# Performance work log

Hardware: AMD Instinct MI355X
Metric: run time of the kernel (lower is better)

## Reference

```python
import jax, jax.numpy as jnp
import numpy as np

N, C_IN, T, V = 64, 64, 64, 25
C_OUT = 64
DK = DV = 16
NH = 8
DKH, DVH = DK // NH, DV // NH
KT = 9
EPS = 1e-5


def make_pe(channel, joint_num, time_len):
    # temporal positional encoding: position index = frame id, repeated per joint
    pos = np.repeat(np.arange(time_len), joint_num).astype(np.float32)[:, None]
    pe = np.zeros((time_len * joint_num, channel), np.float32)
    div = np.exp(np.arange(0, channel, 2).astype(np.float32) * -(np.log(10000.0) / channel))
    pe[:, 0::2] = np.sin(pos * div)
    pe[:, 1::2] = np.cos(pos * div)
    return jnp.asarray(pe.reshape(time_len, joint_num, channel).transpose(2, 0, 1)[None])  # (1,C,time,joint)


def setup_inputs():
    key = jax.random.key(0)
    ks = jax.random.split(key, 17)
    rn = lambda k, s, sc=0.05: jax.random.normal(k, s, jnp.float32) * sc
    return {
        'x': jax.random.normal(ks[0], (N, C_IN, T, V), jnp.float32),
        'pe': make_pe(C_IN, V, 64),
        'data_bn_g': 1.0 + rn(ks[1], (C_IN * V,)),
        'data_bn_b': rn(ks[2], (C_IN * V,)),
        'qkv_w': rn(ks[3], (3 * DK + DV, C_IN), 0.1),
        'qkv_b': rn(ks[4], (3 * DK + DV,)),
        'attn_w': rn(ks[5], (DV, DV), 0.1),
        'attn_b': rn(ks[6], (DV,)),
        'tcn_w': rn(ks[7], (C_OUT - DV, C_IN, KT, 1), 0.05),
        'tcn_b': rn(ks[8], (C_OUT - DV,)),
        'tcn_bn_g': 1.0 + rn(ks[9], (C_OUT - DV,)),
        'tcn_bn_b': rn(ks[10], (C_OUT - DV,)),
        'fc1_w': rn(ks[11], (C_OUT // 2, C_OUT), 0.1),
        'fc1_b': rn(ks[12], (C_OUT // 2,)),
        'fc2_w': rn(ks[13], (C_OUT, C_OUT // 2), 0.1),
        'fc2_b': rn(ks[14], (C_OUT,)),
        'bn_g': 1.0 + rn(ks[15], (C_OUT,)),
        'bn_b': rn(ks[16], (C_OUT,)),
    }


def _bn_eval(x, g, b, axis=1):
    # eval-mode BatchNorm with running_mean=0, running_var=1
    shape = [1] * x.ndim
    shape[axis] = -1
    scale = g / jnp.sqrt(1.0 + EPS)
    return x * scale.reshape(shape) + b.reshape(shape)


def _qkv_heads(x2d, qkv_w, qkv_b):
    # x2d: (B, C, T); 1x1 conv == channel matmul; split q/k/g/v, g is projected but unused
    qkv = jnp.einsum('oc,bct->bot', qkv_w, x2d) + qkv_b[None, :, None]
    q, k, _g, v = jnp.split(qkv, [DK, 2 * DK, 3 * DK], axis=1)
    B = x2d.shape[0]
    split = lambda z, ch: z.reshape(B, NH, ch // NH, -1)  # (B, Nh, chh, T)
    q = split(q, DK) * (DKH ** -0.5)
    return q, split(k, DK), split(v, DV)


def reference(x, pe, data_bn_g, data_bn_b, qkv_w, qkv_b, attn_w, attn_b,
              tcn_w, tcn_b, tcn_bn_g, tcn_bn_b, fc1_w, fc1_b, fc2_w, fc2_b, bn_g, bn_b):
    y = x + pe[:, :, :T]                                 # positional encoding (N,C,T,V)
    x_sum = x
    # data_bn over flattened (C*V) channels
    xb = x.transpose(0, 1, 3, 2).reshape(N, C_IN * V, T)
    xb = _bn_eval(xb, data_bn_g, data_bn_b)
    xn = xb.reshape(N, C_IN, V, T).transpose(0, 1, 3, 2)  # (N,C,T,V)
    # fold joints into batch: (N*V, C, T)
    xf = xn.transpose(0, 3, 1, 2).reshape(N * V, C_IN, T)
    yf = y.transpose(0, 3, 1, 2).reshape(N * V, C_IN, T)
    fq, fk, fv = _qkv_heads(xf, qkv_w, qkv_b)
    pq, pk, _ = _qkv_heads(yf, qkv_w, qkv_b)
    mu_q = fq.mean(-1, keepdims=True)                     # (B,H,dkh,1)
    fqc = fq - mu_q
    logits_pos = jnp.einsum('bhcs,bhct->bhst', pq, pk)    # (B,H,T,T)
    pairwise = jnp.einsum('bhcs,bhct->bhst', fqc, fk)     # (B,H,T,T)
    unary = jnp.einsum('bhcs,bhct->bhst', mu_q, fk)       # (B,H,1,T)
    weights = jnp.tanh(pairwise + logits_pos) + jnp.tanh(unary + logits_pos)
    ao = jnp.einsum('bhst,bhct->bhsc', weights, fv)       # (B,H,T,dvh)
    # (B,H,1,T,dvh) -> permute(0,1,4,2,3) -> combine heads -> (B, DV, T)
    ao = ao.transpose(0, 1, 3, 2).reshape(N * V, DV, T)
    ao = jnp.einsum('oc,bct->bot', attn_w, ao) + attn_b[None, :, None]
    ao = ao.reshape(N, V, DV, T).transpose(0, 2, 3, 1)    # (N, DV, T, V)
    # temporal conv branch (Unit2D: conv(k=9 temporal) + eval BN)
    tc = jax.lax.conv_general_dilated(x_sum, tcn_w, (1, 1), ((KT // 2, KT // 2), (0, 0)),
                                      dimension_numbers=('NCHW', 'OIHW', 'NCHW'))
    tc = tc + tcn_b[None, :, None, None]
    tc = _bn_eval(tc, tcn_bn_g, tcn_bn_b)
    result = jnp.concatenate([tc, ao], axis=1) + x_sum    # residual (down is None)
    # SE-style channel gating
    se = result.mean(axis=(2, 3))                         # (N, C_OUT)
    gate = jax.nn.sigmoid(jax.nn.relu(se @ fc1_w.T + fc1_b) @ fc2_w.T + fc2_b)
    result = result * gate[:, :, None, None] + result
    result = _bn_eval(result, bn_g, bn_b)
    return jax.nn.relu(result)
```

## Files before the change

kernel.cpp:

```cpp
#include <hip/hip_runtime.h>
#include <hip/hip_bf16.h>
#include <math.h>

#define TV_ 1600
#define SCALE_K 2.885390081777927f
#define RS2_ 0.70710678118654752f

typedef __attribute__((ext_vector_type(8))) short bf16x8;
typedef __attribute__((ext_vector_type(4))) float f32x4;
typedef __attribute__((ext_vector_type(2))) __fp16 h2f;

__device__ __forceinline__ float tanh_scaled(float y) {
    y = fminf(44.f, fmaxf(-44.f, y));
    float e = __builtin_amdgcn_exp2f(y);
    float r = __builtin_amdgcn_rcpf(e + 1.f);
    return __builtin_fmaf(e, r, -r);
}

__device__ __forceinline__ ushort f2bf(float f) {
    __hip_bfloat16 h = __float2bfloat16(f);
    return *(ushort*)&h;
}
__device__ __forceinline__ float bf2f(ushort u) {
    uint w = ((uint)u) << 16;
    return __uint_as_float(w);
}

__global__ __launch_bounds__(256) void t1_kernel(
    const float* __restrict__ x, const float* __restrict__ pe,
    const float* __restrict__ tcn_w, const float* __restrict__ tg,
    const float* __restrict__ qkv_w, const float* __restrict__ qkv_b,
    ushort* __restrict__ rt, float* __restrict__ Sbuf, float* __restrict__ Tt,
    ushort* __restrict__ wb, ushort* __restrict__ wq, float* __restrict__ qb,
    ushort* __restrict__ pet)
{
    const int tid = threadIdx.x;
    const int bx = blockIdx.x, by = blockIdx.y;

    if (bx == 25) {
        #pragma unroll 1
        for (int j = 0; j < 9; ++j) {
            int idx = by * 256 + tid + j * 16384;
            if (idx < 27648) {
                int oc = idx / 576, kk = idx - oc * 576;
                int kt = kk >> 6, ci = kk & 63;
                float a = tg[oc] * rsqrtf(1.f + 1e-5f);
                wb[idx] = f2bf(tcn_w[(oc * 64 + ci) * 9 + kt] * a);
            } else if (idx < 32768) {
                int i2 = idx - 27648;
                int r = i2 >> 6, c = i2 & 63;
                int src; float sc;
                if (r < 16)      { src = r;      sc = RS2_; }
                else if (r < 32) { src = r;      sc = SCALE_K; }
                else if (r < 48) { src = r + 16; sc = 1.f; }
                else if (r < 64) { src = r - 48; sc = RS2_; }
                else             { src = r - 48; sc = SCALE_K; }
                wq[i2] = f2bf(qkv_w[src * 64 + c] * sc);
            } else if (idx < 32848) {
                int r = idx - 32768;
                int src; float sc;
                if (r < 16)      { src = r;      sc = RS2_; }
                else if (r < 32) { src = r;      sc = SCALE_K; }
                else if (r < 48) { src = r + 16; sc = 1.f; }
                else if (r < 64) { src = r - 48; sc = RS2_; }
                else             { src = r - 48; sc = SCALE_K; }
                qb[r] = qkv_b[src] * sc;
            } else if (idx < 135248) {
                int i3 = idx - 32848;
                int ci = i3 / 1600, tv = i3 - ci * 1600;
                pet[tv * 64 + ci] = f2bf(pe[ci * 1600 + tv]);
            }
        }
        return;
    }
    if (bx == 26) {
        const int n = by;
        #pragma unroll
        for (int it = 0; it < 2; ++it) {
            int item = tid + it * 256;
            int ci = item >> 3, slot = item & 7;
            int t = (slot < 4) ? slot : (56 + slot);
            const float* xp = x + (n * 64 + ci) * TV_ + t * 25;
            float s = 0.f;
            #pragma unroll
            for (int v = 0; v < 25; ++v) s += xp[v];
            Tt[(n * 64 + ci) * 8 + slot] = s;
        }
        return;
    }

    __shared__ ushort smt[64 * 66];
    const int tv0 = bx * 64;
    const int n = by;
    const int tvl = tid & 63, cig = tid >> 6;
    const int tv = tv0 + tvl;

    float psum[16];
    #pragma unroll
    for (int k = 0; k < 16; ++k) psum[k] = 0.f;
    #pragma unroll
    for (int k = 0; k < 16; ++k) {
        int ci = k * 4 + cig;
        float xv = x[(n * 64 + ci) * TV_ + tv];
        smt[tvl * 66 + ci] = f2bf(xv);
        psum[k] += xv;
    }
    #pragma unroll
    for (int k = 0; k < 16; ++k) {
        float s = psum[k];
        #pragma unroll
        for (int off = 32; off >= 1; off >>= 1) s += __shfl_down(s, off, 64);
        if (tvl == 0) atomicAdd(&Sbuf[n * 64 + k * 4 + cig], s);
    }
    __syncthreads();

    #pragma unroll
    for (int j = 0; j < 8; ++j) {
        int chunk = tid + j * 256;
        int tvr = chunk >> 5, p = chunk & 31;
        uint val = *(const uint*)&smt[tvr * 66 + p * 2];
        *(uint*)&rt[(n * TV_ + tv0 + tvr) * 64 + p * 2] = val;
    }
}

__global__ __launch_bounds__(256, 5) void score_kernel(
    const ushort* __restrict__ rt, const ushort* __restrict__ pet,
    const float* __restrict__ dbg, const float* __restrict__ dbb,
    const ushort* __restrict__ wq, const float* __restrict__ qb,
    const float* __restrict__ attn_w, const float* __restrict__ attn_b,
    float* __restrict__ aoc, float* __restrict__ se)
{
    __shared__ float sm[5312];
    ushort* smu = (ushort*)sm;
    const int MU_ = 1056, AO = 1120;
    const int FKP = 2400, PKP = 2976, FVP = 3552, PQP = 4128, FQP = 4704;

    const int b = blockIdx.x;
    const int l = b >> 3;
    const int n = (b & 7) * 8 + l / 25;
    const int v = l % 25;
    const int tid = threadIdx.x;

    const int lane = tid & 63, wave = tid >> 6;
    const int m16 = lane & 15, q = lane >> 4;

    {
        const int part = tid & 7;
        const int ci0 = part * 8;
        const float rs = rsqrtf(1.f + 1e-5f);
        float sc8[8], sh8[8];
        #pragma unroll
        for (int i = 0; i < 8; ++i) {
            sc8[i] = dbg[(ci0 + i) * 25 + v] * rs;
            sh8[i] = dbb[(ci0 + i) * 25 + v];
        }
        #pragma unroll
        for (int j = 0; j < 2; ++j) {
            int t = (tid + j * 256) >> 3;
            uint4 xr = *(const uint4*)&rt[(n * TV_ + t * 25 + v) * 64 + ci0];
            uint4 pr = *(const uint4*)&pet[(t * 25 + v) * 64 + ci0];
            const ushort* xu = (const ushort*)&xr;
            const ushort* pu = (const ushort*)&pr;
            ushort xs[8], ys[8];
            #pragma unroll
            for (int i = 0; i < 8; ++i) {
                float xf = bf2f(xu[i]);
                xs[i] = f2bf(xf * sc8[i] + sh8[i]);
                ys[i] = f2bf(xf + bf2f(pu[i]));
            }
            *(uint4*)&smu[t * 72 + ci0] = *(uint4*)xs;
            *(uint4*)&smu[4608 + t * 72 + ci0] = *(uint4*)ys;
        }
    }
    __syncthreads();

    f32x4 acc[5];
    #pragma unroll
    for (int mt = 0; mt < 5; ++mt) acc[mt] = (f32x4){0.f, 0.f, 0.f, 0.f};
    #pragma unroll
    for (int kt = 0; kt < 2; ++kt) {
        const int koff = kt * 32 + q * 8;
        bf16x8 bx = *(const bf16x8*)&smu[(wave * 16 + m16) * 72 + koff];
        bf16x8 by = *(const bf16x8*)&smu[4608 + (wave * 16 + m16) * 72 + koff];
        #pragma unroll
        for (int mt = 0; mt < 5; ++mt) {
            bf16x8 a = *(const bf16x8*)&wq[(mt * 16 + m16) * 64 + koff];
            acc[mt] = __builtin_amdgcn_mfma_f32_16x16x32_bf16(a, (mt < 3) ? bx : by, acc[mt], 0, 0, 0);
        }
    }
    __syncthreads();

    {
        const int t = wave * 16 + m16;
        #pragma unroll
        for (int r = 0; r < 4; ++r)
            sm[(q * 4 + r) * 66 + t] = acc[0][r] + qb[q * 4 + r];
        *(h2f*)&sm[FKP + t * 9 + 2 * q] =
            __builtin_amdgcn_cvt_pkrtz(acc[1][0] + qb[16 + q * 4], acc[1][1] + qb[16 + q * 4 + 1]);
        *(h2f*)&sm[FKP + t * 9 + 2 * q + 1] =
            __builtin_amdgcn_cvt_pkrtz(acc[1][2] + qb[16 + q * 4 + 2], acc[1][3] + qb[16 + q * 4 + 3]);
        *(h2f*)&sm[FVP + t * 9 + 2 * q] =
            __builtin_amdgcn_cvt_pkrtz(acc[2][0] + qb[32 + q * 4], acc[2][1] + qb[32 + q * 4 + 1]);
        *(h2f*)&sm[FVP + t * 9 + 2 * q + 1] =
            __builtin_amdgcn_cvt_pkrtz(acc[2][2] + qb[32 + q * 4 + 2], acc[2][3] + qb[32 + q * 4 + 3]);
        *(h2f*)&sm[PQP + t * 9 + 2 * q] =
            __builtin_amdgcn_cvt_pkrtz(acc[3][0] + qb[48 + q * 4], acc[3][1] + qb[48 + q * 4 + 1]);
        *(h2f*)&sm[PQP + t * 9 + 2 * q + 1] =
            __builtin_amdgcn_cvt_pkrtz(acc[3][2] + qb[48 + q * 4 + 2], acc[3][3] + qb[48 + q * 4 + 3]);
        *(h2f*)&sm[PKP + t * 9 + 2 * q] =
            __builtin_amdgcn_cvt_pkrtz(acc[4][0] + qb[64 + q * 4], acc[4][1] + qb[64 + q * 4 + 1]);
        *(h2f*)&sm[PKP + t * 9 + 2 * q + 1] =
            __builtin_amdgcn_cvt_pkrtz(acc[4][2] + qb[64 + q * 4 + 2], acc[4][3] + qb[64 + q * 4 + 3]);
    }
    __syncthreads();

    if (tid < 64) {
        int ch = tid & 15, qq = tid >> 4;
        float s = 0.f;
        #pragma unroll
        for (int t = 0; t < 16; ++t) s += sm[ch * 66 + qq * 16 + t];
        sm[MU_ + qq * 16 + ch] = s;
    }
    __syncthreads();
    if (tid < 16) {
        float mval = (sm[MU_ + tid] + sm[MU_ + 16 + tid] + sm[MU_ + 32 + tid] + sm[MU_ + 48 + tid]) * (1.f / 64.f);
        sm[MU_ + tid] = mval;
    }
    __syncthreads();

    #pragma unroll
    for (int e = 0; e < 2; ++e) {
        int idx = tid * 2 + e;
        int s = idx >> 3, h = idx & 7;
        float a = sm[(2 * h) * 66 + s] - sm[MU_ + 2 * h];
        float c = sm[(2 * h + 1) * 66 + s] - sm[MU_ + 2 * h + 1];
        *(h2f*)&sm[FQP + s * 9 + h] = __builtin_amdgcn_cvt_pkrtz(a, c);
    }
    __syncthreads();

    const int g3 = tid & 7, m3 = tid >> 3;
    #pragma unroll 1
    for (int h = 0; h < 8; ++h) {
        const float mu0 = sm[MU_ + 2 * h], mu1 = sm[MU_ + 2 * h + 1];
        float fq0c[2], fq1c[2], pq0[2], pq1[2];
        #pragma unroll
        for (int js = 0; js < 2; ++js) {
            int s = 2 * m3 + js;
            h2f fq2 = *(const h2f*)&sm[FQP + s * 9 + h];
            h2f pq2 = *(const h2f*)&sm[PQP + s * 9 + h];
            fq0c[js] = (float)fq2.x; fq1c[js] = (float)fq2.y;
            pq0[js] = (float)pq2.x;  pq1[js] = (float)pq2.y;
        }
        float ao00 = 0.f, ao01 = 0.f, ao10 = 0.f, ao11 = 0.f;
        #pragma unroll
        for (int ch = 0; ch < 2; ++ch) {
            float fk0[4], fk1[4], pk0[4], pk1[4], fv0[4], fv1[4], un[4];
            #pragma unroll
            for (int j = 0; j < 4; ++j) {
                int t = 8 * g3 + ch * 4 + j;
                h2f fk2 = *(const h2f*)&sm[FKP + t * 9 + h];
                h2f pk2 = *(const h2f*)&sm[PKP + t * 9 + h];
                h2f fv2 = *(const h2f*)&sm[FVP + t * 9 + h];
                fk0[j] = (float)fk2.x; fk1[j] = (float)fk2.y;
                pk0[j] = (float)pk2.x; pk1[j] = (float)pk2.y;
                fv0[j] = (float)fv2.x; fv1[j] = (float)fv2.y;
                un[j] = mu0 * fk0[j] + mu1 * fk1[j];
            }
            #pragma unroll
            for (int js = 0; js < 2; ++js) {
                #pragma unroll
                for (int j = 0; j < 4; ++j) {
                    float lp = pq0[js] * pk0[j] + pq1[js] * pk1[j];
                    float a1 = fq0c[js] * fk0[j] + fq1c[js] * fk1[j] + lp;
                    float a2 = un[j] + lp;
                    float w = tanh_scaled(a1) + tanh_scaled(a2);
                    if (js == 0) { ao00 += w * fv0[j]; ao01 += w * fv1[j]; }
                    else         { ao10 += w * fv0[j]; ao11 += w * fv1[j]; }
                }
            }
        }
        #pragma unroll
        for (int off = 1; off <= 4; off <<= 1) {
            ao00 += __shfl_xor(ao00, off);
            ao01 += __shfl_xor(ao01, off);
            ao10 += __shfl_xor(ao10, off);
            ao11 += __shfl_xor(ao11, off);
        }
        if (g3 == 0) {
            sm[AO + (2 * m3) * 20 + 2 * h]         = ao00;
            sm[AO + (2 * m3) * 20 + 2 * h + 1]     = ao01;
            sm[AO + (2 * m3 + 1) * 20 + 2 * h]     = ao10;
            sm[AO + (2 * m3 + 1) * 20 + 2 * h + 1] = ao11;
        }
    }
    __syncthreads();

    const int t = tid & 63, oq = tid >> 6;
    float aorow[16];
    #pragma unroll
    for (int i = 0; i < 4; ++i)
        *(float4*)&aorow[i * 4] = *(const float4*)&sm[AO + t * 20 + i * 4];
    float* aop = aoc + (n * 25 + v) * 1024;
    #pragma unroll
    for (int j = 0; j < 4; ++j) {
        int o = oq * 4 + j;
        float acc4 = attn_b[o];
        #pragma unroll
        for (int c = 0; c < 16; ++c) acc4 += attn_w[o * 16 + c] * aorow[c];
        aop[o * 64 + t] = acc4;
        float ssum = acc4;
        #pragma unroll
        for (int off = 32; off >= 1; off >>= 1) ssum += __shfl_down(ssum, off, 64);
        if ((tid & 63) == 0) atomicAdd(&se[n * 64 + 48 + o], ssum);
    }
}

__global__ __launch_bounds__(64) void gate_kernel(
    const float* __restrict__ se, const float* __restrict__ Sbuf,
    const float* __restrict__ Tt, const ushort* __restrict__ wb,
    const float* __restrict__ tcn_b, const float* __restrict__ tg,
    const float* __restrict__ tb,
    const float* __restrict__ fc1w, const float* __restrict__ fc1b,
    const float* __restrict__ fc2w, const float* __restrict__ fc2b,
    float* __restrict__ gate)
{
    const int n = blockIdx.x;
    const int tid = threadIdx.x;
    __shared__ float U[64][9], seL[64], hid[32];
    const float rs = rsqrtf(1.f + 1e-5f);

    {
        int ci = tid;
        float S = Sbuf[n * 64 + ci];
        float T[8];
        #pragma unroll
        for (int j = 0; j < 8; ++j) T[j] = Tt[(n * 64 + ci) * 8 + j];
        U[ci][0] = S - (T[4] + T[5] + T[6] + T[7]);
        U[ci][1] = S - (T[5] + T[6] + T[7]);
        U[ci][2] = S - (T[6] + T[7]);
        U[ci][3] = S - T[7];
        U[ci][4] = S;
        U[ci][5] = S - T[0];
        U[ci][6] = S - (T[0] + T[1]);
        U[ci][7] = S - (T[0] + T[1] + T[2]);
        U[ci][8] = S - (T[0] + T[1] + T[2] + T[3]);
    }
    __syncthreads();

    if (tid < 48) {
        int oc = tid;
        float cs = 0.f;
        #pragma unroll 1
        for (int kt = 0; kt < 9; ++kt) {
            #pragma unroll
            for (int cb = 0; cb < 8; ++cb) {
                bf16x8 w8 = *(const bf16x8*)&wb[oc * 576 + kt * 64 + cb * 8];
                #pragma unroll
                for (int i = 0; i < 8; ++i)
                    cs += bf2f((ushort)w8[i]) * U[cb * 8 + i][kt];
            }
        }
        float a = tg[oc] * rs;
        float cb_ = tcn_b[oc] * a + tb[oc];
        seL[oc] = (a * cs + 1600.f * cb_ + Sbuf[n * 64 + oc]) * (1.f / 1600.f);
    } else {
        seL[tid] = (se[n * 64 + tid] + Sbuf[n * 64 + tid]) * (1.f / 1600.f);
    }
    __syncthreads();
    if (tid < 32) {
        float a = fc1b[tid];
        #pragma unroll
        for (int c = 0; c < 64; ++c) a += fc1w[tid * 64 + c] * seL[c];
        hid[tid] = fmaxf(a, 0.f);
    }
    __syncthreads();
    float g = fc2b[tid];
    #pragma unroll
    for (int j = 0; j < 32; ++j) g += fc2w[tid * 32 + j] * hid[j];
    gate[n * 64 + tid] = 1.f / (1.f + __expf(-g));
}

__global__ __launch_bounds__(512, 1) void tcn_mfma_kernel(
    const ushort* __restrict__ rt, const float* __restrict__ x,
    const ushort* __restrict__ wb,
    const float* __restrict__ tcn_b, const float* __restrict__ tg,
    const float* __restrict__ tb, const float* __restrict__ gate,
    const float* __restrict__ bng, const float* __restrict__ bnb,
    float* __restrict__ out)
{
    __shared__ ushort xsl[600 * 72];
    const int b = blockIdx.x;
    const int n = b >> 2, tile = b & 3;
    const int t0 = tile * 16;
    const int tid = threadIdx.x;

    const int tvbase = (t0 - 4) * 25;
    for (int idx = tid; idx < 4800; idx += 512) {
        int r = idx >> 3, part = idx & 7;
        int tv = tvbase + r;
        uint4 val = make_uint4(0u, 0u, 0u, 0u);
        if (tv >= 0 && tv < TV_) val = *(const uint4*)&rt[(n * TV_ + tv) * 64 + part * 8];
        *(uint4*)&xsl[r * 72 + part * 8] = val;
    }
    __syncthreads();

    const int lane = tid & 63, wave = tid >> 6;
    const int m16 = lane & 15, q = lane >> 4;
    const int nt0 = wave * 3;

    f32x4 acc[3][3];
    f32x4 acc24[3];
    #pragma unroll
    for (int i = 0; i < 3; ++i)
        #pragma unroll
        for (int mt = 0; mt < 3; ++mt)
            acc[i][mt] = (f32x4){0.f, 0.f, 0.f, 0.f};
    #pragma unroll
    for (int mt = 0; mt < 3; ++mt) acc24[mt] = (f32x4){0.f, 0.f, 0.f, 0.f};

    for (int ktile = 0; ktile < 18; ++ktile) {
        const int kt = ktile >> 1;
        const int cib = (ktile & 1) * 32 + q * 8;
        bf16x8 afr[3];
        #pragma unroll
        for (int mt = 0; mt < 3; ++mt)
            afr[mt] = *(const bf16x8*)&wb[(mt * 16 + m16) * 576 + ktile * 32 + q * 8];
        #pragma unroll
        for (int i = 0; i < 3; ++i) {
            int p = (nt0 + i) * 16 + m16;
            bf16x8 bfr = *(const bf16x8*)&xsl[(p + kt * 25) * 72 + cib];
            #pragma unroll
            for (int mt = 0; mt < 3; ++mt)
                acc[i][mt] = __builtin_amdgcn_mfma_f32_16x16x32_bf16(afr[mt], bfr, acc[i][mt], 0, 0, 0);
        }
        if (wave == 0) {
            int p = 24 * 16 + m16;
            bf16x8 bfr = *(const bf16x8*)&xsl[(p + kt * 25) * 72 + cib];
            #pragma unroll
            for (int mt = 0; mt < 3; ++mt)
                acc24[mt] = __builtin_amdgcn_mfma_f32_16x16x32_bf16(afr[mt], bfr, acc24[mt], 0, 0, 0);
        }
    }

    const float rsbn = rsqrtf(1.f + 1e-5f);
    float cb3[3][4], m3_[3][4], bb3[3][4];
    #pragma unroll
    for (int mt = 0; mt < 3; ++mt)
        #pragma unroll
        for (int r = 0; r < 4; ++r) {
            int oc = mt * 16 + q * 4 + r;
            float a = tg[oc] * rsbn;
            cb3[mt][r] = tcn_b[oc] * a + tb[oc];
            m3_[mt][r] = (1.f + gate[n * 64 + oc]) * (bng[oc] * rsbn);
            bb3[mt][r] = bnb[oc];
        }
    #pragma unroll
    for (int i = 0; i < 3; ++i) {
        int posg = tile * 400 + (nt0 + i) * 16 + m16;
        #pragma unroll
        for (int mt = 0; mt < 3; ++mt) {
            #pragma unroll
            for (int r = 0; r < 4; ++r) {
                int oc = mt * 16 + q * 4 + r;
                float val = acc[i][mt][r] + cb3[mt][r] + x[(n * 64 + oc) * TV_ + posg];
                out[(n * 64 + oc) * TV_ + posg] = fmaxf(val * m3_[mt][r] + bb3[mt][r], 0.f);
            }
        }
    }
    if (wave == 0) {
        int posg = tile * 400 + 24 * 16 + m16;
        #pragma unroll
        for (int mt = 0; mt < 3; ++mt) {
            #pragma unroll
            for (int r = 0; r < 4; ++r) {
                int oc = mt * 16 + q * 4 + r;
                float val = acc24[mt][r] + cb3[mt][r] + x[(n * 64 + oc) * TV_ + posg];
                out[(n * 64 + oc) * TV_ + posg] = fmaxf(val * m3_[mt][r] + bb3[mt][r], 0.f);
            }
        }
    }
}

__global__ __launch_bounds__(256) void final_kernel(
    float* __restrict__ out, const float* __restrict__ aoc,
    const float* __restrict__ x, const float* __restrict__ gate,
    const float* __restrict__ bng, const float* __restrict__ bnb)
{
    const float rs = rsqrtf(1.f + 1e-5f);
    int idx = blockIdx.x * 256 + threadIdx.x;
    int n = idx / 6400;
    int rem = idx - n * 6400;
    int o = rem / 400, r4 = rem - o * 400;

    float4 val;
    const float* ap = aoc + (n * 25) * 1024 + o * 64;
    #pragma unroll
    for (int e = 0; e < 4; ++e) {
        int pos = r4 * 4 + e;
        int t = pos / 25, v = pos - t * 25;
        ((float*)&val)[e] = ap[v * 1024 + t];
    }
    int g4 = (n * 64 + 48 + o) * 400 + r4;
    float4 xr = ((const float4*)x)[g4];
    float mm = (1.f + gate[n * 64 + 48 + o]) * (bng[48 + o] * rs);
    float bb = bnb[48 + o];
    val.x = fmaxf((val.x + xr.x) * mm + bb, 0.f);
    val.y = fmaxf((val.y + xr.y) * mm + bb, 0.f);
    val.z = fmaxf((val.z + xr.z) * mm + bb, 0.f);
    val.w = fmaxf((val.w + xr.w) * mm + bb, 0.f);
    ((float4*)out)[g4] = val;
}

extern "C" void kernel_launch(void* const* d_in, const int* in_sizes, int n_in,
                              void* d_out, int out_size, void* d_ws, size_t ws_size,
                              hipStream_t stream) {
    const float* x     = (const float*)d_in[0];
    const float* pe    = (const float*)d_in[1];
    const float* dbg   = (const float*)d_in[2];
    const float* dbb   = (const float*)d_in[3];
    const float* qkvw  = (const float*)d_in[4];
    const float* qkvb  = (const float*)d_in[5];
    const float* attnw = (const float*)d_in[6];
    const float* attnb = (const float*)d_in[7];
    const float* tcnw  = (const float*)d_in[8];
    const float* tcnb  = (const float*)d_in[9];
    const float* tcng  = (const float*)d_in[10];
    const float* tcnbb = (const float*)d_in[11];
    const float* fc1w  = (const float*)d_in[12];
    const float* fc1b  = (const float*)d_in[13];
    const float* fc2w  = (const float*)d_in[14];
    const float* fc2b  = (const float*)d_in[15];
    const float* bng   = (const float*)d_in[16];
    const float* bnb   = (const float*)d_in[17];

    float* out  = (float*)d_out;
    float* se   = (float*)d_ws;
    float* Sbuf = se + 4096;
    float* Tt   = Sbuf + 4096;
    float* gate = Tt + 32768;
    float* qb   = gate + 4096;
    float* aoc  = qb + 96;
    ushort* wb  = (ushort*)(aoc + 1638400);
    ushort* wq  = wb + 27648;
    ushort* pet = wq + 5120;
    ushort* rt  = pet + 102400;

    hipMemsetAsync(se, 0, (4096 + 4096) * sizeof(float), stream);
    t1_kernel<<<dim3(27, 64), dim3(256), 0, stream>>>(
        x, pe, tcnw, tcng, qkvw, qkvb, rt, Sbuf, Tt, wb, wq, qb, pet);
    score_kernel<<<dim3(1600), dim3(256), 0, stream>>>(rt, pet, dbg, dbb, wq, qb, attnw, attnb, aoc, se);
    gate_kernel<<<dim3(64), dim3(64), 0, stream>>>(
        se, Sbuf, Tt, wb, tcnb, tcng, tcnbb, fc1w, fc1b, fc2w, fc2b, gate);
    tcn_mfma_kernel<<<dim3(256), dim3(512), 0, stream>>>(
        rt, x, wb, tcnb, tcng, tcnbb, gate, bng, bnb, out);
    final_kernel<<<dim3(1600), dim3(256), 0, stream>>>(out, aoc, x, gate, bng, bnb);
}
```

Measured before the change: 226.0 us.

## Fuse SE gate computation into TCN kernel and stage attention output through LDS

Removes the separate gate_kernel launch by computing the SE gate redundantly inside each tcn_mfma block, splitting the 48x9 weight dot products across 432 threads, with tile 0 writing the gate out for the final kernel. The final kernel now handles one (n, channel) pair per block and first loads the aoc rows coalesced into shared memory before transposing, replacing strided global gathers. The score kernel's occupancy hint is raised from 5 to 6. This trades one launch and uncoalesced reads for four-fold redundant gate work per sample and extra LDS use in the TCN kernel.

```diff
diff --git a/kernel.cpp b/kernel.cpp
--- a/kernel.cpp
+++ b/kernel.cpp
@@ -123,7 +123,7 @@
     }
 }
 
-__global__ __launch_bounds__(256, 5) void score_kernel(
+__global__ __launch_bounds__(256, 6) void score_kernel(
     const ushort* __restrict__ rt, const ushort* __restrict__ pet,
     const float* __restrict__ dbg, const float* __restrict__ dbb,
     const ushort* __restrict__ wq, const float* __restrict__ qb,
@@ -315,84 +315,28 @@
     }
 }
 
-__global__ __launch_bounds__(64) void gate_kernel(
-    const float* __restrict__ se, const float* __restrict__ Sbuf,
-    const float* __restrict__ Tt, const ushort* __restrict__ wb,
-    const float* __restrict__ tcn_b, const float* __restrict__ tg,
-    const float* __restrict__ tb,
-    const float* __restrict__ fc1w, const float* __restrict__ fc1b,
-    const float* __restrict__ fc2w, const float* __restrict__ fc2b,
-    float* __restrict__ gate)
-{
-    const int n = blockIdx.x;
-    const int tid = threadIdx.x;
-    __shared__ float U[64][9], seL[64], hid[32];
-    const float rs = rsqrtf(1.f + 1e-5f);
-
-    {
-        int ci = tid;
-        float S = Sbuf[n * 64 + ci];
-        float T[8];
-        #pragma unroll
-        for (int j = 0; j < 8; ++j) T[j] = Tt[(n * 64 + ci) * 8 + j];
-        U[ci][0] = S - (T[4] + T[5] + T[6] + T[7]);
-        U[ci][1] = S - (T[5] + T[6] + T[7]);
-        U[ci][2] = S - (T[6] + T[7]);
-        U[ci][3] = S - T[7];
-        U[ci][4] = S;
-        U[ci][5] = S - T[0];
-        U[ci][6] = S - (T[0] + T[1]);
-        U[ci][7] = S - (T[0] + T[1] + T[2]);
-        U[ci][8] = S - (T[0] + T[1] + T[2] + T[3]);
-    }
-    __syncthreads();
-
-    if (tid < 48) {
-        int oc = tid;
-        float cs = 0.f;
-        #pragma unroll 1
-        for (int kt = 0; kt < 9; ++kt) {
-            #pragma unroll
-            for (int cb = 0; cb < 8; ++cb) {
-                bf16x8 w8 = *(const bf16x8*)&wb[oc * 576 + kt * 64 + cb * 8];
-                #pragma unroll
-                for (int i = 0; i < 8; ++i)
-                    cs += bf2f((ushort)w8[i]) * U[cb * 8 + i][kt];
-            }
-        }
-        float a = tg[oc] * rs;
-        float cb_ = tcn_b[oc] * a + tb[oc];
-        seL[oc] = (a * cs + 1600.f * cb_ + Sbuf[n * 64 + oc]) * (1.f / 1600.f);
-    } else {
-        seL[tid] = (se[n * 64 + tid] + Sbuf[n * 64 + tid]) * (1.f / 1600.f);
-    }
-    __syncthreads();
-    if (tid < 32) {
-        float a = fc1b[tid];
-        #pragma unroll
-        for (int c = 0; c < 64; ++c) a += fc1w[tid * 64 + c] * seL[c];
-        hid[tid] = fmaxf(a, 0.f);
-    }
-    __syncthreads();
-    float g = fc2b[tid];
-    #pragma unroll
-    for (int j = 0; j < 32; ++j) g += fc2w[tid * 32 + j] * hid[j];
-    gate[n * 64 + tid] = 1.f / (1.f + __expf(-g));
-}
-
 __global__ __launch_bounds__(512, 1) void tcn_mfma_kernel(
     const ushort* __restrict__ rt, const float* __restrict__ x,
     const ushort* __restrict__ wb,
     const float* __restrict__ tcn_b, const float* __restrict__ tg,
-    const float* __restrict__ tb, const float* __restrict__ gate,
+    const float* __restrict__ tb,
+    const float* __restrict__ se, const float* __restrict__ Sbuf,
+    const float* __restrict__ Tt,
+    const float* __restrict__ fc1w, const float* __restrict__ fc1b,
+    const float* __restrict__ fc2w, const float* __restrict__ fc2b,
     const float* __restrict__ bng, const float* __restrict__ bnb,
-    float* __restrict__ out)
+    float* __restrict__ gate_out, float* __restrict__ out)
 {
     __shared__ ushort xsl[600 * 72];
+    __shared__ float U[576];
+    __shared__ float gpart[432];
+    __shared__ float seL[64], hid[32], gateL[64];
+
     const int b = blockIdx.x;
     const int n = b >> 2, tile = b & 3;
     const int t0 = tile * 16;
     const int tid = threadIdx.x;
+    const float rsbn = rsqrtf(1.f + 1e-5f);
 
     const int tvbase = (t0 - 4) * 25;
     for (int idx = tid; idx < 4800; idx += 512) {
@@ -402,6 +346,64 @@
         if (tv >= 0 && tv < TV_) val = *(const uint4*)&rt[(n * TV_ + tv) * 64 + part * 8];
         *(uint4*)&xsl[r * 72 + part * 8] = val;
     }
+
+    if (tid < 64) {
+        float S = Sbuf[n * 64 + tid];
+        float T[8];
+        #pragma unroll
+        for (int j = 0; j < 8; ++j) T[j] = Tt[(n * 64 + tid) * 8 + j];
+        U[tid * 9 + 0] = S - (T[4] + T[5] + T[6] + T[7]);
+        U[tid * 9 + 1] = S - (T[5] + T[6] + T[7]);
+        U[tid * 9 + 2] = S - (T[6] + T[7]);
+        U[tid * 9 + 3] = S - T[7];
+        U[tid * 9 + 4] = S;
+        U[tid * 9 + 5] = S - T[0];
+        U[tid * 9 + 6] = S - (T[0] + T[1]);
+        U[tid * 9 + 7] = S - (T[0] + T[1] + T[2]);
+        U[tid * 9 + 8] = S - (T[0] + T[1] + T[2] + T[3]);
+    }
+    __syncthreads();
+    if (tid < 432) {
+        int oc = tid / 9, kt = tid - oc * 9;
+        float cs = 0.f;
+        #pragma unroll
+        for (int cb = 0; cb < 8; ++cb) {
+            bf16x8 w8 = *(const bf16x8*)&wb[oc * 576 + kt * 64 + cb * 8];
+            #pragma unroll
+            for (int i = 0; i < 8; ++i)
+                cs += bf2f((ushort)w8[i]) * U[(cb * 8 + i) * 9 + kt];
+        }
+        gpart[tid] = cs;
+    }
+    __syncthreads();
+    if (tid < 64) {
+        if (tid < 48) {
+            float cs = 0.f;
+            #pragma unroll
+            for (int kt = 0; kt < 9; ++kt) cs += gpart[tid * 9 + kt];
+            float a = tg[tid] * rsbn;
+            float cb_ = tcn_b[tid] * a + tb[tid];
+            seL[tid] = (a * cs + 1600.f * cb_ + Sbuf[n * 64 + tid]) * (1.f / 1600.f);
+        } else {
+            seL[tid] = (se[n * 64 + tid] + Sbuf[n * 64 + tid]) * (1.f / 1600.f);
+        }
+    }
+    __syncthreads();
+    if (tid < 32) {
+        float a = fc1b[tid];
+        #pragma unroll
+        for (int c = 0; c < 64; ++c) a += fc1w[tid * 64 + c] * seL[c];
+        hid[tid] = fmaxf(a, 0.f);
+    }
+    __syncthreads();
+    if (tid < 64) {
+        float g = fc2b[tid];
+        #pragma unroll
+        for (int j = 0; j < 32; ++j) g += fc2w[tid * 32 + j] * hid[j];
+        float gv = 1.f / (1.f + __expf(-g));
+        gateL[tid] = gv;
+        if (tile == 0) gate_out[n * 64 + tid] = gv;
+    }
     __syncthreads();
 
     const int lane = tid & 63, wave = tid >> 6;
@@ -442,7 +444,6 @@
         }
     }
 
-    const float rsbn = rsqrtf(1.f + 1e-5f);
     float cb3[3][4], m3_[3][4], bb3[3][4];
     #pragma unroll
     for (int mt = 0; mt < 3; ++mt)
@@ -451,7 +452,7 @@
             int oc = mt * 16 + q * 4 + r;
             float a = tg[oc] * rsbn;
             cb3[mt][r] = tcn_b[oc] * a + tb[oc];
-            m3_[mt][r] = (1.f + gate[n * 64 + oc]) * (bng[oc] * rsbn);
+            m3_[mt][r] = (1.f + gateL[oc]) * (bng[oc] * rsbn);
             bb3[mt][r] = bnb[oc];
         }
     #pragma unroll
@@ -486,29 +487,37 @@
     const float* __restrict__ x, const float* __restrict__ gate,
     const float* __restrict__ bng, const float* __restrict__ bnb)
 {
+    __shared__ float ts[25 * 68];
+    const int bx = blockIdx.x;
+    const int o = bx & 15, n = bx >> 4;
+    const int tid = threadIdx.x;
     const float rs = rsqrtf(1.f + 1e-5f);
-    int idx = blockIdx.x * 256 + threadIdx.x;
-    int n = idx / 6400;
-    int rem = idx - n * 6400;
-    int o = rem / 400, r4 = rem - o * 400;
-
-    float4 val;
-    const float* ap = aoc + (n * 25) * 1024 + o * 64;
-    #pragma unroll
-    for (int e = 0; e < 4; ++e) {
-        int pos = r4 * 4 + e;
-        int t = pos / 25, v = pos - t * 25;
-        ((float*)&val)[e] = ap[v * 1024 + t];
-    }
-    int g4 = (n * 64 + 48 + o) * 400 + r4;
-    float4 xr = ((const float4*)x)[g4];
-    float mm = (1.f + gate[n * 64 + 48 + o]) * (bng[48 + o] * rs);
-    float bb = bnb[48 + o];
-    val.x = fmaxf((val.x + xr.x) * mm + bb, 0.f);
-    val.y = fmaxf((val.y + xr.y) * mm + bb, 0.f);
-    val.z = fmaxf((val.z + xr.z) * mm + bb, 0.f);
-    val.w = fmaxf((val.w + xr.w) * mm + bb, 0.f);
-    ((float4*)out)[g4] = val;
+
+    for (int task = tid; task < 400; task += 256) {
+        int v = task >> 4, f = task & 15;
+        float4 d = *(const float4*)&aoc[(n * 25 + v) * 1024 + o * 64 + f * 4];
+        *(float4*)&ts[v * 68 + f * 4] = d;
+    }
+    __syncthreads();
+
+    const float mm = (1.f + gate[n * 64 + 48 + o]) * (bng[48 + o] * rs);
+    const float bb = bnb[48 + o];
+    const int base4 = (n * 64 + 48 + o) * 400;
+    for (int p4 = tid; p4 < 400; p4 += 256) {
+        float4 xr = ((const float4*)x)[base4 + p4];
+        float4 val;
+        #pragma unroll
+        for (int e = 0; e < 4; ++e) {
+            int pos = p4 * 4 + e;
+            int t = pos / 25, v = pos - t * 25;
+            ((float*)&val)[e] = ts[v * 68 + t];
+        }
+        val.x = fmaxf((val.x + xr.x) * mm + bb, 0.f);
+        val.y = fmaxf((val.y + xr.y) * mm + bb, 0.f);
+        val.z = fmaxf((val.z + xr.z) * mm + bb, 0.f);
+        val.w = fmaxf((val.w + xr.w) * mm + bb, 0.f);
+        ((float4*)out)[base4 + p4] = val;
+    }
 }
 
 extern "C" void kernel_launch(void* const* d_in, const int* in_sizes, int n_in,
@@ -549,9 +558,8 @@
     t1_kernel<<<dim3(27, 64), dim3(256), 0, stream>>>(
         x, pe, tcnw, tcng, qkvw, qkvb, rt, Sbuf, Tt, wb, wq, qb, pet);
     score_kernel<<<dim3(1600), dim3(256), 0, stream>>>(rt, pet, dbg, dbb, wq, qb, attnw, attnb, aoc, se);
-    gate_kernel<<<dim3(64), dim3(64), 0, stream>>>(
-        se, Sbuf, Tt, wb, tcnb, tcng, tcnbb, fc1w, fc1b, fc2w, fc2b, gate);
     tcn_mfma_kernel<<<dim3(256), dim3(512), 0, stream>>>(
-        rt, x, wb, tcnb, tcng, tcnbb, gate, bng, bnb, out);
-    final_kernel<<<dim3(1600), dim3(256), 0, stream>>>(out, aoc, x, gate, bng, bnb);
-}
+        rt, x, wb, tcnb, tcng, tcnbb, se, Sbuf, Tt,
+        fc1w, fc1b, fc2w, fc2b, bng, bnb, gate, out);
+    final_kernel<<<dim3(1024), dim3(256), 0, stream>>>(out, aoc, x, gate, bng, bnb);
+}
```

After: 220.0 us. -2.7%, faster.
